# Kernel optimization log

Measured on AMD Instinct MI355X. Metric: run time of the kernel, lower is better.

Reference implementation:

```python
import jax, jax.numpy as jnp
import numpy as np

N, E, G = 50000, 1600000, 64          # nodes, edges, graphs
NODE_IN, EDGE_IN, HID, L, H = 32, 16, 64, 3, 4
C = HID // H                           # per-head channels (PyG out_channels)


def setup_inputs() -> dict:
    key = jax.random.key(0)
    ks = jax.random.split(key, 12)
    x = jax.random.normal(ks[0], (N, NODE_IN), jnp.float32)
    edge_index = jax.random.randint(ks[1], (2, E), 0, N, jnp.int32)
    edge_attr = jax.random.normal(ks[2], (E, EDGE_IN), jnp.float32)
    batch = jnp.sort(jax.random.randint(ks[3], (N,), 0, G, jnp.int32))
    s = lambda k, shape, fan: jax.random.normal(k, shape, jnp.float32) / np.sqrt(fan)
    Wn = s(ks[4], (NODE_IN, HID), NODE_IN); bn = jnp.zeros((HID,), jnp.float32)
    Wq = s(ks[5], (L, HID, HID), HID);      bq = jnp.zeros((L, HID), jnp.float32)
    Wk = s(ks[6], (L, HID, HID), HID);      bk = jnp.zeros((L, HID), jnp.float32)
    Wv = s(ks[7], (L, HID, HID), HID);      bv = jnp.zeros((L, HID), jnp.float32)
    We = s(ks[8], (L, EDGE_IN, HID), EDGE_IN)          # lin_edge, bias=False in PyG
    Ws = s(ks[9], (L, HID, HID), HID);      bs = jnp.zeros((L, HID), jnp.float32)  # lin_skip
    W1 = s(ks[10], (HID, HID // 2), HID);   b1 = jnp.zeros((HID // 2,), jnp.float32)
    W2 = s(ks[11], (HID // 2, 1), HID // 2); b2 = jnp.zeros((1,), jnp.float32)
    return dict(x=x, edge_index=edge_index, edge_attr=edge_attr, batch=batch,
                Wn=Wn, bn=bn, Wq=Wq, bq=bq, Wk=Wk, bk=bk, Wv=Wv, bv=bv,
                We=We, Ws=Ws, bs=bs, W1=W1, b1=b1, W2=W2, b2=b2)


def _transformer_conv(x, src, dst, edge_attr, Wq, bq, Wk, bk, Wv, bv, We, Ws, bs):
    # PyG TransformerConv (concat=True, beta=False, root_weight=True), eval mode.
    q = (x @ Wq + bq)[dst].reshape(E, H, C)              # query at target nodes
    e = (edge_attr @ We).reshape(E, H, C)                # edge embedding
    k = (x @ Wk + bk)[src].reshape(E, H, C) + e          # key at source + edge
    alpha = (q * k).sum(-1) / jnp.sqrt(jnp.float32(C))   # [E, H]
    amax = jax.ops.segment_max(alpha, dst, num_segments=N)
    ex = jnp.exp(alpha - amax[dst])
    denom = jax.ops.segment_sum(ex, dst, num_segments=N)
    attn = ex / (denom[dst] + 1e-16)                     # segment softmax over in-edges
    v = (x @ Wv + bv)[src].reshape(E, H, C) + e
    agg = jax.ops.segment_sum((v * attn[..., None]).reshape(E, HID), dst, num_segments=N)
    return agg + x @ Ws + bs                             # skip connection (lin_skip)


def reference(x, edge_index, edge_attr, batch, Wn, bn, Wq, bq, Wk, bk, Wv, bv,
              We, Ws, bs, W1, b1, W2, b2):
    src, dst = edge_index[0], edge_index[1]
    h = jax.nn.relu(x @ Wn + bn)
    for l in range(L):  # dropout is identity in eval mode
        h_new = jax.nn.relu(_transformer_conv(h, src, dst, edge_attr,
                                              Wq[l], bq[l], Wk[l], bk[l],
                                              Wv[l], bv[l], We[l], Ws[l], bs[l]))
        h = h + h_new
    # global_mean_pool
    cnt = jax.ops.segment_sum(jnp.ones((N,), h.dtype), batch, num_segments=G)
    pooled = jax.ops.segment_sum(h, batch, num_segments=G) / jnp.maximum(cnt, 1.0)[:, None]
    out = jax.nn.relu(pooled @ W1 + b1) @ W2 + b2
    return out.squeeze(-1)
```

## Files before the change

kernel.cpp:

```cpp
#include <hip/hip_runtime.h>
#include <hip/hip_fp16.h>
#include <stdint.h>

#define Nn 50000
#define Ee 1600000
#define Gg 64
#define TB 2048
#define NTB ((Ee + TB - 1) / TB)
#define NBK ((Nn + 255) / 256)

__global__ void k_hist(const int* __restrict__ ei, int* __restrict__ deg) {
    int e = blockIdx.x * blockDim.x + threadIdx.x;
    if (e < Ee) atomicAdd(&deg[ei[Ee + e]], 1);
}

__global__ void k_scan1(const int* __restrict__ deg, int* __restrict__ row_ptr,
                        int* __restrict__ bsum) {
    __shared__ int buf[256];
    int i = blockIdx.x * 256 + threadIdx.x;
    int v = (i < Nn) ? deg[i] : 0;
    buf[threadIdx.x] = v;
    __syncthreads();
    for (int off = 1; off < 256; off <<= 1) {
        int t = (threadIdx.x >= off) ? buf[threadIdx.x - off] : 0;
        __syncthreads();
        buf[threadIdx.x] += t;
        __syncthreads();
    }
    if (i < Nn) row_ptr[i + 1] = buf[threadIdx.x];
    if (threadIdx.x == 255) bsum[blockIdx.x] = buf[255];
}

__global__ void k_scan2(int* __restrict__ bsum, int nb) {
    __shared__ int buf[256];
    int v = (threadIdx.x < nb) ? bsum[threadIdx.x] : 0;
    buf[threadIdx.x] = v;
    __syncthreads();
    for (int off = 1; off < 256; off <<= 1) {
        int t = (threadIdx.x >= off) ? buf[threadIdx.x - off] : 0;
        __syncthreads();
        buf[threadIdx.x] += t;
        __syncthreads();
    }
    if (threadIdx.x < nb) bsum[threadIdx.x] = buf[threadIdx.x];
}

__global__ void k_scan3(int* __restrict__ row_ptr, const int* __restrict__ bsum) {
    int i = blockIdx.x * 256 + threadIdx.x;
    if (i > Nn) return;
    if (i == 0) { row_ptr[0] = 0; return; }
    int b = (i - 1) >> 8;
    if (b > 0) row_ptr[i] += bsum[b - 1];
}

__global__ void k_scatter(const int* __restrict__ ei, int* __restrict__ cursor,
                          int* __restrict__ src_perm, int* __restrict__ eperm) {
    int e = blockIdx.x * blockDim.x + threadIdx.x;
    if (e >= Ee) return;
    int dst = ei[Ee + e];
    int pos = atomicAdd(&cursor[dst], 1);
    src_perm[pos] = ei[e];
    eperm[pos] = e;
}

__global__ void k_easort(const float* __restrict__ ea, const int* __restrict__ eperm,
                         __half* __restrict__ ea_h) {
    long t = (long)blockIdx.x * blockDim.x + threadIdx.x;
    if (t >= (long)Ee * 4) return;
    long idx = t >> 2;
    int e = eperm[idx];
    float4 v = ((const float4*)ea)[(long)e * 4 + (t & 3)];
    __half2 lo = __floats2half2_rn(v.x, v.y);
    __half2 hi = __floats2half2_rn(v.z, v.w);
    ((__half2*)ea_h)[t * 2]     = lo;
    ((__half2*)ea_h)[t * 2 + 1] = hi;
}


__global__ __launch_bounds__(256) void k_cnt(const int* __restrict__ ei,
                                             int* __restrict__ table) {
    __shared__ int hist[NBK];
    for (int i = threadIdx.x; i < NBK; i += 256) hist[i] = 0;
    __syncthreads();
    int e0 = blockIdx.x * TB;
    for (int i = threadIdx.x; i < TB; i += 256) {
        int e = e0 + i;
        if (e >= Ee) break;
        atomicAdd(&hist[ei[Ee + e] >> 8], 1);
    }
    __syncthreads();
    for (int i = threadIdx.x; i < NBK; i += 256)
        table[i * NTB + blockIdx.x] = hist[i];
}

__global__ __launch_bounds__(256) void k_colscan(int* __restrict__ table,
                                                 int* __restrict__ bktsz) {
    __shared__ int buf[1024];
    int c = blockIdx.x;
    for (int k = 0; k < 4; ++k) {
        int i = threadIdx.x + k * 256;
        buf[i] = (i < NTB) ? table[c * NTB + i] : 0;
    }
    __syncthreads();
    for (int off = 1; off < 1024; off <<= 1) {
        int v[4];
        for (int k = 0; k < 4; ++k) {
            int i = threadIdx.x + k * 256;
            v[k] = (i >= off) ? buf[i - off] : 0;
        }
        __syncthreads();
        for (int k = 0; k < 4; ++k) buf[threadIdx.x + k * 256] += v[k];
        __syncthreads();
    }
    for (int k = 0; k < 4; ++k) {
        int i = threadIdx.x + k * 256;
        if (i < NTB) table[c * NTB + i] = i ? buf[i - 1] : 0;
    }
    if (threadIdx.x == 0) bktsz[c] = buf[1023];
}

__global__ __launch_bounds__(256) void k_bktscan(const int* __restrict__ bktsz,
                                                 int* __restrict__ bktbase) {
    __shared__ int buf[256];
    int i = threadIdx.x;
    buf[i] = (i < NBK) ? bktsz[i] : 0;
    __syncthreads();
    for (int off = 1; off < 256; off <<= 1) {
        int v = (i >= off) ? buf[i - off] : 0;
        __syncthreads();
        buf[i] += v;
        __syncthreads();
    }
    if (i == 0) bktbase[0] = 0;
    if (i < NBK) bktbase[i + 1] = buf[i];
}

__global__ __launch_bounds__(256) void k_binfill(const int* __restrict__ ei,
                        const int* __restrict__ table, const int* __restrict__ bktbase,
                        unsigned long long* __restrict__ tmp) {
    __shared__ int off_s[NBK];
    __shared__ int cnt_s[NBK];
    for (int i = threadIdx.x; i < NBK; i += 256) {
        off_s[i] = table[i * NTB + blockIdx.x];
        cnt_s[i] = 0;
    }
    __syncthreads();
    int e0 = blockIdx.x * TB;
    for (int i = threadIdx.x; i < TB; i += 256) {
        int e = e0 + i;
        if (e >= Ee) break;
        int src = ei[e];
        int dst = ei[Ee + e];
        int b = dst >> 8;
        int r = atomicAdd(&cnt_s[b], 1);
        long pos = (long)bktbase[b] + off_s[b] + r;
        tmp[pos] = ((unsigned long long)(unsigned)dst << 37)
                 | ((unsigned long long)(unsigned)src << 21)
                 | (unsigned long long)(unsigned)e;
    }
}

__global__ __launch_bounds__(256) void k_bktB(const unsigned long long* __restrict__ tmp,
                        const int* __restrict__ bktbase, int* __restrict__ row_ptr,
                        unsigned long long* __restrict__ tmp2) {
    __shared__ int cnt[256];
    __shared__ int sc[256];
    __shared__ int lro[256];
    int b = blockIdx.x, tid = threadIdx.x;
    cnt[tid] = 0;
    __syncthreads();
    int s = bktbase[b], t_end = bktbase[b + 1];
    for (int i = s + tid; i < t_end; i += 256)
        atomicAdd(&cnt[(int)(tmp[i] >> 37) & 255], 1);
    __syncthreads();
    sc[tid] = cnt[tid];
    __syncthreads();
    for (int off = 1; off < 256; off <<= 1) {
        int v = (tid >= off) ? sc[tid - off] : 0;
        __syncthreads();
        sc[tid] += v;
        __syncthreads();
    }
    lro[tid] = tid ? sc[tid - 1] : 0;
    cnt[tid] = 0;
    int n = b * 256 + tid;
    if (n < Nn) row_ptr[n] = s + lro[tid];
    if (b == NBK - 1 && tid == 0) row_ptr[Nn] = Ee;
    __syncthreads();
    for (int i = s + tid; i < t_end; i += 256) {
        unsigned long long p = tmp[i];
        int dn = (int)(p >> 37) & 255;
        int r = atomicAdd(&cnt[dn], 1);
        int pos = s + lro[dn] + r;
        tmp2[pos] = (((p >> 21) & 0xFFFFull) << 32) | (p & 0x1FFFFFull);
    }
}

__global__ void k_scatB(const unsigned long long* __restrict__ tmp2,
                        int* __restrict__ src_perm,
                        const float* __restrict__ ea, __half* __restrict__ ea_h) {
    int t = blockIdx.x * blockDim.x + threadIdx.x;
    if (t >= Ee) return;
    unsigned long long p = tmp2[t];
    src_perm[t] = (int)(p >> 32);
    int e = (int)(p & 0xFFFFFFFFull);
    const float4* er = (const float4*)(ea + (size_t)e * 16);
    float4 v0 = er[0], v1 = er[1], v2 = er[2], v3 = er[3];
    __half2 h0 = __floats2half2_rn(v0.x, v0.y), h1 = __floats2half2_rn(v0.z, v0.w);
    __half2 h2 = __floats2half2_rn(v1.x, v1.y), h3 = __floats2half2_rn(v1.z, v1.w);
    __half2 h4 = __floats2half2_rn(v2.x, v2.y), h5 = __floats2half2_rn(v2.z, v2.w);
    __half2 h6 = __floats2half2_rn(v3.x, v3.y), h7 = __floats2half2_rn(v3.z, v3.w);
    uint4 a = make_uint4(*(unsigned*)&h0, *(unsigned*)&h1,
                         *(unsigned*)&h2, *(unsigned*)&h3);
    uint4 bb = make_uint4(*(unsigned*)&h4, *(unsigned*)&h5,
                          *(unsigned*)&h6, *(unsigned*)&h7);
    uint4* o = (uint4*)(ea_h + (size_t)t * 16);
    o[0] = a;
    o[1] = bb;
}

__global__ void k_gbound(const int* __restrict__ batch, int* __restrict__ gstart) {
    int n = blockIdx.x * blockDim.x + threadIdx.x;
    if (n >= Nn) return;
    int b = batch[n];
    if (n == 0) { for (int g = 0; g <= b; ++g) gstart[g] = 0; }
    else { int bp = batch[n - 1]; for (int g = bp + 1; g <= b; ++g) gstart[g] = n; }
    if (n == Nn - 1) { for (int g = b + 1; g <= Gg; ++g) gstart[g] = Nn; }
}

__global__ __launch_bounds__(256) void k_encode(const float* __restrict__ x,
                         const float* __restrict__ Wn,
                         const float* __restrict__ bn, float* __restrict__ h) {
    __shared__ float sx[64 * 32];
    int base = blockIdx.x * 64;
    for (int i = threadIdx.x; i < 512; i += 256) {
        int off = i * 4, row = off >> 5;
        float4 v = (base + row < Nn) ? ((const float4*)(x))[(base * 32 + off) >> 2]
                                     : make_float4(0.f, 0.f, 0.f, 0.f);
        ((float4*)sx)[i] = v;
    }
    __syncthreads();
    int lane = threadIdx.x & 63, wv = threadIdx.x >> 6;
    float acc[16];
    float b = bn[lane];
#pragma unroll
    for (int nn = 0; nn < 16; ++nn) acc[nn] = b;
#pragma unroll 1
    for (int k0 = 0; k0 < 32; k0 += 4) {
        float w0 = Wn[(k0 + 0) * 64 + lane];
        float w1 = Wn[(k0 + 1) * 64 + lane];
        float w2 = Wn[(k0 + 2) * 64 + lane];
        float w3 = Wn[(k0 + 3) * 64 + lane];
#pragma unroll
        for (int nn = 0; nn < 16; ++nn) {
            int row = wv * 16 + nn;
            float4 hv = *(const float4*)&sx[row * 32 + k0];
            acc[nn] = fmaf(hv.x, w0, fmaf(hv.y, w1, fmaf(hv.z, w2, fmaf(hv.w, w3, acc[nn]))));
        }
    }
#pragma unroll
    for (int nn = 0; nn < 16; ++nn) {
        int n = base + wv * 16 + nn;
        if (n < Nn) h[(size_t)n * 64 + lane] = fmaxf(acc[nn], 0.f);
    }
}

__global__ void k_wqm3(const float* __restrict__ Wq_all, const float* __restrict__ bq_all,
                       const float* __restrict__ We_all, float* __restrict__ Wqm3,
                       float* __restrict__ bqm3) {
    int l = blockIdx.x;
    const float* Wq = Wq_all + l * 4096;
    const float* bq = bq_all + l * 64;
    const float* We = We_all + l * 1024;
    float* Wqm = Wqm3 + l * 4096;
    float* bqm = bqm3 + l * 64;
    for (int o = threadIdx.x; o < 64 * 64; o += 256) {
        int j = o >> 6, lp = o & 63, hh = lp >> 4, ii = lp & 15;
        float acc = 0.f;
#pragma unroll
        for (int c = 0; c < 16; ++c)
            acc += Wq[j * 64 + hh * 16 + c] * We[ii * 64 + hh * 16 + c];
        Wqm[o] = acc;
    }
    if (threadIdx.x < 64) {
        int hh = threadIdx.x >> 4, ii = threadIdx.x & 15;
        float acc = 0.f;
#pragma unroll
        for (int c = 0; c < 16; ++c)
            acc += bq[hh * 16 + c] * We[ii * 64 + hh * 16 + c];
        bqm[threadIdx.x] = acc;
    }
}

__global__ __launch_bounds__(256) void k_qkvt(const float* __restrict__ h,
                       const float* __restrict__ Wq, const float* __restrict__ bq,
                       const float* __restrict__ Wk, const float* __restrict__ bk,
                       const float* __restrict__ Wv, const float* __restrict__ bv,
                       const float* __restrict__ Wqm, const float* __restrict__ bqm,
                       const float* __restrict__ Ws, const float* __restrict__ bs,
                       float* __restrict__ qn, __half* __restrict__ kv,
                       float* __restrict__ tq, float* __restrict__ sn) {
    __shared__ float sh[64 * 64];
    int base = blockIdx.x * 64;
    for (int i = threadIdx.x; i < 1024; i += 256) {
        int off = i * 4, row = off >> 6;
        float4 v = (base + row < Nn) ? ((const float4*)(h))[((size_t)base * 64 + off) >> 2]
                                     : make_float4(0.f, 0.f, 0.f, 0.f);
        ((float4*)sh)[i] = v;
    }
    __syncthreads();
    int lane = threadIdx.x & 63, wv = threadIdx.x >> 6;
    float aq[16], ak[16], av[16], at[16], as_[16];
    float _bq = bq[lane], _bk = bk[lane], _bv = bv[lane], _bt = bqm[lane], _bs = bs[lane];
#pragma unroll
    for (int nn = 0; nn < 16; ++nn) {
        aq[nn] = _bq; ak[nn] = _bk; av[nn] = _bv; at[nn] = _bt; as_[nn] = _bs;
    }
#pragma unroll 1
    for (int k0 = 0; k0 < 64; k0 += 4) {
        float wq[4], wk[4], wvv[4], wt[4], ws[4];
#pragma unroll
        for (int j = 0; j < 4; ++j) {
            wq[j] = Wq[(k0 + j) * 64 + lane];
            wk[j] = Wk[(k0 + j) * 64 + lane];
            wvv[j] = Wv[(k0 + j) * 64 + lane];
            wt[j] = Wqm[(k0 + j) * 64 + lane];
            ws[j] = Ws[(k0 + j) * 64 + lane];
        }
#pragma unroll
        for (int nn = 0; nn < 16; ++nn) {
            int row = wv * 16 + nn;
            float4 hv = *(const float4*)&sh[row * 64 + k0];
            aq[nn] = fmaf(hv.x, wq[0], fmaf(hv.y, wq[1], fmaf(hv.z, wq[2], fmaf(hv.w, wq[3], aq[nn]))));
            ak[nn] = fmaf(hv.x, wk[0], fmaf(hv.y, wk[1], fmaf(hv.z, wk[2], fmaf(hv.w, wk[3], ak[nn]))));
            av[nn] = fmaf(hv.x, wvv[0], fmaf(hv.y, wvv[1], fmaf(hv.z, wvv[2], fmaf(hv.w, wvv[3], av[nn]))));
            at[nn] = fmaf(hv.x, wt[0], fmaf(hv.y, wt[1], fmaf(hv.z, wt[2], fmaf(hv.w, wt[3], at[nn]))));
            as_[nn] = fmaf(hv.x, ws[0], fmaf(hv.y, ws[1], fmaf(hv.z, ws[2], fmaf(hv.w, ws[3], as_[nn]))));
        }
    }
#pragma unroll
    for (int nn = 0; nn < 16; ++nn) {
        int n = base + wv * 16 + nn;
        if (n < Nn) {
            size_t o = (size_t)n * 64 + lane;
            qn[o] = aq[nn]; tq[o] = at[nn]; sn[o] = as_[nn];
            kv[(size_t)n * 128 + lane]      = __float2half_rn(ak[nn]);
            kv[(size_t)n * 128 + 64 + lane] = __float2half_rn(av[nn]);
        }
    }
}

__global__ __launch_bounds__(256) void k_layer2(float* __restrict__ h,
                      const float* __restrict__ qn, const __half* __restrict__ kv,
                      const float* __restrict__ tq, const float* __restrict__ sn,
                      const int* __restrict__ row_ptr, const int* __restrict__ src_perm,
                      const __half* __restrict__ eah, const float* __restrict__ We) {
    __shared__ float sWe[1024];
    __shared__ float tE[4][64];
    __shared__ float tV[4][64];
    for (int t = threadIdx.x; t < 1024; t += 256) sWe[t] = We[t];
    __syncthreads();
    int lane = threadIdx.x & 63, wv = threadIdx.x >> 6;
    int slot = lane >> 5, sl = lane & 31;
    int n = blockIdx.x * 4 + wv;
    if (n >= Nn) return;
    int beg = row_ptr[n], end = row_ptr[n + 1];
    const float SC = 0.25f * 1.4426950408889634f;
    float2 q2 = *(const float2*)&qn[(size_t)n * 64 + 2 * sl];
    float2 t2 = *(const float2*)&tq[(size_t)n * 64 + 2 * sl];
    q2.x *= SC; q2.y *= SC; t2.x *= SC; t2.y *= SC;
    const __half2* kv2 = (const __half2*)kv;
    const __half2* ea2 = (const __half2*)eah;
    float m = -INFINITY, accd = 0.f;
    float2 accv = make_float2(0.f, 0.f), acce = make_float2(0.f, 0.f);
    for (int idx = beg; idx < end; idx += 4) {
        int e0 = idx + slot, e1 = idx + 2 + slot;
        bool ok0 = e0 < end, ok1 = e1 < end;
        int i0 = ok0 ? e0 : beg, i1 = ok1 ? e1 : beg;
        int s0 = src_perm[i0], s1 = src_perm[i1];
        float2 k0 = __half22float2(kv2[s0 * 64 + sl]);
        float2 v0 = __half22float2(kv2[s0 * 64 + 32 + sl]);
        float2 k1 = __half22float2(kv2[s1 * 64 + sl]);
        float2 v1 = __half22float2(kv2[s1 * 64 + 32 + sl]);
        float2 x0 = __half22float2(ea2[(size_t)i0 * 8 + (sl & 7)]);
        float2 x1 = __half22float2(ea2[(size_t)i1 * 8 + (sl & 7)]);
        float a0 = fmaf(q2.x, k0.x, fmaf(q2.y, k0.y, fmaf(t2.x, x0.x, t2.y * x0.y)));
        float a1 = fmaf(q2.x, k1.x, fmaf(q2.y, k1.y, fmaf(t2.x, x1.x, t2.y * x1.y)));
        a0 += __shfl_xor(a0, 1, 8); a1 += __shfl_xor(a1, 1, 8);
        a0 += __shfl_xor(a0, 2, 8); a1 += __shfl_xor(a1, 2, 8);
        a0 += __shfl_xor(a0, 4, 8); a1 += __shfl_xor(a1, 4, 8);
        if (!ok0) a0 = -INFINITY;
        if (!ok1) a1 = -INFINITY;
        float b0 = __shfl_xor(a0, 32), b1 = __shfl_xor(a1, 32);
        float nm = fmaxf(m, fmaxf(fmaxf(a0, b0), fmaxf(a1, b1)));
        float w = __builtin_exp2f(m - nm);
        float p0 = __builtin_exp2f(a0 - nm), p1 = __builtin_exp2f(a1 - nm);
        accd = fmaf(accd, w, p0 + p1);
        accv.x = fmaf(accv.x, w, fmaf(p0, v0.x, p1 * v1.x));
        accv.y = fmaf(accv.y, w, fmaf(p0, v0.y, p1 * v1.y));
        acce.x = fmaf(acce.x, w, fmaf(p0, x0.x, p1 * x1.x));
        acce.y = fmaf(acce.y, w, fmaf(p0, x0.y, p1 * x1.y));
        m = nm;
    }
    accd   += __shfl_xor(accd, 32);
    accv.x += __shfl_xor(accv.x, 32);
    accv.y += __shfl_xor(accv.y, 32);
    acce.x += __shfl_xor(acce.x, 32);
    acce.y += __shfl_xor(acce.y, 32);
    float inv = 1.f / (accd + 1e-16f);
    if (slot == 0) {
        ((float2*)tE[wv])[sl] = make_float2(acce.x * inv, acce.y * inv);
        ((float2*)tV[wv])[sl] = make_float2(accv.x * inv, accv.y * inv);
    }
    int hh = lane >> 4;
    float re = 0.f;
#pragma unroll
    for (int i = 0; i < 16; ++i)
        re = fmaf(tE[wv][hh * 16 + i], sWe[i * 64 + lane], re);
    size_t o = (size_t)n * 64 + lane;
    float hv = h[o];
    h[o] = hv + fmaxf(tV[wv][lane] + re + sn[o], 0.f);
}

template <bool SORTED>
__global__ __launch_bounds__(256) void k_layer(float* __restrict__ h,
                      const float* __restrict__ qn, const __half* __restrict__ kv,
                      const float* __restrict__ tq, const float* __restrict__ sn,
                      const int* __restrict__ row_ptr, const int* __restrict__ src_perm,
                      const int* __restrict__ eperm, const __half* __restrict__ eah,
                      const float* __restrict__ eaf, const float* __restrict__ We) {
    __shared__ float sWe[1024];
    __shared__ float tile[4][64];
    for (int t = threadIdx.x; t < 1024; t += 256) sWe[t] = We[t];
    __syncthreads();
    int lane = threadIdx.x & 63, wv = threadIdx.x >> 6;
    int hh = lane >> 4, cc = lane & 15;
    int n = blockIdx.x * 4 + wv;
    if (n >= Nn) return;
    int beg = row_ptr[n], end = row_ptr[n + 1];
    const float SC = 0.25f * 1.4426950408889634f;
    float q = qn[(size_t)n * 64 + lane] * SC;
    float t = tq[(size_t)n * 64 + lane] * SC;
    float m = -INFINITY, accd = 0.f, accv = 0.f, acce = 0.f;
    int idx = beg;
    for (; idx < end; ++idx) {
        long b0 = (long)src_perm[idx] * 128;
        float k0 = __half2float(kv[b0 + lane]);
        float v0 = __half2float(kv[b0 + 64 + lane]);
        float x0 = SORTED ? __half2float(eah[(long)idx * 16 + cc])
                          : eaf[(long)eperm[idx] * 16 + cc];
        float a0 = fmaf(q, k0, x0 * t);
        a0 += __shfl_xor(a0, 1, 16);
        a0 += __shfl_xor(a0, 2, 16);
        a0 += __shfl_xor(a0, 4, 16);
        a0 += __shfl_xor(a0, 8, 16);
        float nm = fmaxf(m, a0);
        float w = __builtin_exp2f(m - nm);
        float p0 = __builtin_exp2f(a0 - nm);
        accd = fmaf(accd, w, p0);
        accv = fmaf(accv, w, p0 * v0);
        acce = fmaf(acce, w, p0 * x0);
        m = nm;
    }
    float inv = 1.f / (accd + 1e-16f);
    tile[wv][lane] = acce * inv;
    float re = 0.f;
#pragma unroll
    for (int i = 0; i < 16; ++i)
        re = fmaf(tile[wv][hh * 16 + i], sWe[i * 64 + lane], re);
    size_t o = (size_t)n * 64 + lane;
    float hv = h[o];
    h[o] = hv + fmaxf(fmaf(accv, inv, re + sn[o]), 0.f);
}

__global__ void k_pool(const float* __restrict__ h, const int* __restrict__ gstart,
                       const float* __restrict__ W1, const float* __restrict__ b1,
                       const float* __restrict__ W2, const float* __restrict__ b2,
                       float* __restrict__ out) {
    int g = blockIdx.x;
    int lane = threadIdx.x & 63, wv = threadIdx.x >> 6;
    int beg = gstart[g], end = gstart[g + 1];
    __shared__ float red[4][64];
    __shared__ float sp[64];
    __shared__ float sh[32];
    float acc = 0.f;
    for (int n = beg + wv; n < end; n += 4) acc += h[(size_t)n * 64 + lane];
    red[wv][lane] = acc;
    __syncthreads();
    if (threadIdx.x < 64) {
        float c = fmaxf((float)(end - beg), 1.f);
        sp[lane] = (red[0][lane] + red[1][lane] + red[2][lane] + red[3][lane]) / c;
    }
    __syncthreads();
    if (threadIdx.x < 32) {
        int t = threadIdx.x;
        float a = b1[t];
#pragma unroll
        for (int i = 0; i < 64; ++i) a = fmaf(sp[i], W1[i * 32 + t], a);
        sh[t] = fmaxf(a, 0.f) * W2[t];
    }
    __syncthreads();
    if (threadIdx.x == 0) {
        float s = b2[0];
#pragma unroll
        for (int i = 0; i < 32; ++i) s += sh[i];
        out[g] = s;
    }
}

extern "C" void kernel_launch(void* const* d_in, const int* in_sizes, int n_in,
                              void* d_out, int out_size, void* d_ws, size_t ws_size,
                              hipStream_t stream) {
    const float* x   = (const float*)d_in[0];
    const int*   ei  = (const int*)d_in[1];
    const float* ea  = (const float*)d_in[2];
    const int*   bat = (const int*)d_in[3];
    const float* Wn  = (const float*)d_in[4];
    const float* bn  = (const float*)d_in[5];
    const float* Wq  = (const float*)d_in[6];
    const float* bq  = (const float*)d_in[7];
    const float* Wk  = (const float*)d_in[8];
    const float* bk  = (const float*)d_in[9];
    const float* Wv  = (const float*)d_in[10];
    const float* bv  = (const float*)d_in[11];
    const float* We  = (const float*)d_in[12];
    const float* Wsk = (const float*)d_in[13];
    const float* bs  = (const float*)d_in[14];
    const float* W1  = (const float*)d_in[15];
    const float* b1  = (const float*)d_in[16];
    const float* W2  = (const float*)d_in[17];
    const float* b2  = (const float*)d_in[18];
    float* out = (float*)d_out;

    const size_t NH = (size_t)Nn * 64;
    float* h    = (float*)d_ws;
    float* qn   = h + NH;
    float* tq   = h + 2 * NH;
    float* sn   = h + 3 * NH;
    __half* kv  = (__half*)(h + 4 * NH);
    float* Wqm3 = h + 5 * NH;
    float* bqm3 = Wqm3 + 3 * 4096;
    int* deg       = (int*)(bqm3 + 3 * 64);
    int* row_ptr   = deg + Nn;
    int* cursor    = row_ptr + Nn + 1;
    int* src_perm  = cursor + Nn;
    int* eperm     = src_perm + Ee;
    int* bsum      = eperm + Ee;
    int* gstart    = bsum + 256;
    char* pe = (char*)(gstart + Gg + 1);
    __half* ea_h = (__half*)(((uintptr_t)pe + 63) & ~(uintptr_t)63);
    char* pt = (char*)(ea_h + (size_t)Ee * 16);
    unsigned long long* tmp =
        (unsigned long long*)(((uintptr_t)pt + 15) & ~(uintptr_t)15);
    size_t need_eah = ((char*)(ea_h + (size_t)Ee * 16)) - (char*)d_ws;
    size_t need_tmp = ((char*)(tmp + Ee)) - (char*)d_ws;
    unsigned long long* tmp2 = (unsigned long long*)qn;
    int* table   = (int*)tq;
    int* bktsz   = (int*)sn;
    int* bktbase = bktsz + 256;
    int mode = (ws_size >= need_tmp) ? 2 : (ws_size >= need_eah) ? 1 : 0;

    if (mode == 2) {
        k_cnt<<<NTB, 256, 0, stream>>>(ei, table);
        k_colscan<<<NBK, 256, 0, stream>>>(table, bktsz);
        k_bktscan<<<1, 256, 0, stream>>>(bktsz, bktbase);
        k_binfill<<<NTB, 256, 0, stream>>>(ei, table, bktbase, tmp);
        k_bktB<<<NBK, 256, 0, stream>>>(tmp, bktbase, row_ptr, tmp2);
        k_scatB<<<(Ee + 255) / 256, 256, 0, stream>>>(tmp2, src_perm, ea, ea_h);
    } else {
        const int NB = 196;
        hipMemsetAsync(deg, 0, Nn * sizeof(int), stream);
        k_hist<<<(Ee + 255) / 256, 256, 0, stream>>>(ei, deg);
        k_scan1<<<NB, 256, 0, stream>>>(deg, row_ptr, bsum);
        k_scan2<<<1, 256, 0, stream>>>(bsum, NB);
        k_scan3<<<(Nn + 256) / 256, 256, 0, stream>>>(row_ptr, bsum);
        hipMemcpyAsync(cursor, row_ptr, Nn * sizeof(int), hipMemcpyDeviceToDevice, stream);
        k_scatter<<<(Ee + 255) / 256, 256, 0, stream>>>(ei, cursor, src_perm, eperm);
        if (mode == 1)
            k_easort<<<((long)Ee * 4 + 255) / 256, 256, 0, stream>>>(ea, eperm, ea_h);
    }
    k_gbound<<<(Nn + 255) / 256, 256, 0, stream>>>(bat, gstart);
    k_wqm3<<<3, 256, 0, stream>>>(Wq, bq, We, Wqm3, bqm3);

    int nodeBlocks = (Nn + 63) / 64;
    k_encode<<<nodeBlocks, 256, 0, stream>>>(x, Wn, bn, h);
    for (int l = 0; l < 3; ++l) {
        k_qkvt<<<nodeBlocks, 256, 0, stream>>>(h, Wq + l * 4096, bq + l * 64,
                                               Wk + l * 4096, bk + l * 64,
                                               Wv + l * 4096, bv + l * 64,
                                               Wqm3 + l * 4096, bqm3 + l * 64,
                                               Wsk + l * 4096, bs + l * 64,
                                               qn, kv, tq, sn);
        if (mode >= 1)
            k_layer2<<<(Nn + 3) / 4, 256, 0, stream>>>(h, qn, kv, tq, sn,
                    row_ptr, src_perm, ea_h, We + l * 1024);
        else
            k_layer<false><<<(Nn + 3) / 4, 256, 0, stream>>>(h, qn, kv, tq, sn,
                    row_ptr, src_perm, eperm, ea_h, ea, We + l * 1024);
    }
    k_pool<<<Gg, 256, 0, stream>>>(h, gstart, W1, b1, W2, b2, out);
}
```

Measured before the change: 725.2 us.

## Process eight edges per wave with fp16 dot2 and max-free softmax

Rewrites the per-node attention kernel so each edge uses 16 lanes with 4-wide fp16 loads of key, value and edge features. A wave now handles 8 edges per iteration instead of 4. Attention logits are computed with packed fp16 dot2 instructions on fp16-rounded queries. The online running-max rescaling is replaced by a fixed exponent offset of -6, which removes the max and rescale work per step. In exchange, the scores lose precision and exp2 can overflow or underflow if logits fall far outside the expected range.

```diff
diff --git a/kernel.cpp b/kernel.cpp
--- a/kernel.cpp
+++ b/kernel.cpp
@@ -8,6 +8,17 @@
 #define TB 2048
 #define NTB ((Ee + TB - 1) / TB)
 #define NBK ((Nn + 255) / 256)
+
+typedef _Float16 f16x2 __attribute__((ext_vector_type(2)));
+typedef _Float16 f16x4 __attribute__((ext_vector_type(4)));
+
+__device__ __forceinline__ float fdot2f(f16x2 a, f16x2 b, float c) {
+#if __has_builtin(__builtin_amdgcn_fdot2)
+    return __builtin_amdgcn_fdot2(a, b, c, false);
+#else
+    return fmaf((float)a[0], (float)b[0], fmaf((float)a[1], (float)b[1], c));
+#endif
+}
 
 __global__ void k_hist(const int* __restrict__ ei, int* __restrict__ deg) {
     int e = blockIdx.x * blockDim.x + threadIdx.x;
@@ -350,7 +361,7 @@
     }
 }
 
-__global__ __launch_bounds__(256) void k_layer2(float* __restrict__ h,
+__global__ __launch_bounds__(256) void k_layer4(float* __restrict__ h,
                       const float* __restrict__ qn, const __half* __restrict__ kv,
                       const float* __restrict__ tq, const float* __restrict__ sn,
                       const int* __restrict__ row_ptr, const int* __restrict__ src_perm,
@@ -361,56 +372,69 @@
     for (int t = threadIdx.x; t < 1024; t += 256) sWe[t] = We[t];
     __syncthreads();
     int lane = threadIdx.x & 63, wv = threadIdx.x >> 6;
-    int slot = lane >> 5, sl = lane & 31;
+    int slot = lane >> 4, sl = lane & 15;
     int n = blockIdx.x * 4 + wv;
     if (n >= Nn) return;
     int beg = row_ptr[n], end = row_ptr[n + 1];
     const float SC = 0.25f * 1.4426950408889634f;
-    float2 q2 = *(const float2*)&qn[(size_t)n * 64 + 2 * sl];
-    float2 t2 = *(const float2*)&tq[(size_t)n * 64 + 2 * sl];
-    q2.x *= SC; q2.y *= SC; t2.x *= SC; t2.y *= SC;
-    const __half2* kv2 = (const __half2*)kv;
-    const __half2* ea2 = (const __half2*)eah;
-    float m = -INFINITY, accd = 0.f;
-    float2 accv = make_float2(0.f, 0.f), acce = make_float2(0.f, 0.f);
-    for (int idx = beg; idx < end; idx += 4) {
-        int e0 = idx + slot, e1 = idx + 2 + slot;
+    float4 q4 = *(const float4*)&qn[(size_t)n * 64 + 4 * sl];
+    float4 t4 = *(const float4*)&tq[(size_t)n * 64 + 4 * sl];
+    f16x2 qa = {(_Float16)(q4.x * SC), (_Float16)(q4.y * SC)};
+    f16x2 qb = {(_Float16)(q4.z * SC), (_Float16)(q4.w * SC)};
+    f16x2 ta = {(_Float16)(t4.x * SC), (_Float16)(t4.y * SC)};
+    f16x2 tb = {(_Float16)(t4.z * SC), (_Float16)(t4.w * SC)};
+    const int xoff = 4 * (sl & 3);
+    float accd = 0.f;
+    float4 accv = make_float4(0.f, 0.f, 0.f, 0.f);
+    float4 acce = make_float4(0.f, 0.f, 0.f, 0.f);
+    for (int idx = beg; idx < end; idx += 8) {
+        int e0 = idx + slot, e1 = idx + 4 + slot;
         bool ok0 = e0 < end, ok1 = e1 < end;
         int i0 = ok0 ? e0 : beg, i1 = ok1 ? e1 : beg;
         int s0 = src_perm[i0], s1 = src_perm[i1];
-        float2 k0 = __half22float2(kv2[s0 * 64 + sl]);
-        float2 v0 = __half22float2(kv2[s0 * 64 + 32 + sl]);
-        float2 k1 = __half22float2(kv2[s1 * 64 + sl]);
-        float2 v1 = __half22float2(kv2[s1 * 64 + 32 + sl]);
-        float2 x0 = __half22float2(ea2[(size_t)i0 * 8 + (sl & 7)]);
-        float2 x1 = __half22float2(ea2[(size_t)i1 * 8 + (sl & 7)]);
-        float a0 = fmaf(q2.x, k0.x, fmaf(q2.y, k0.y, fmaf(t2.x, x0.x, t2.y * x0.y)));
-        float a1 = fmaf(q2.x, k1.x, fmaf(q2.y, k1.y, fmaf(t2.x, x1.x, t2.y * x1.y)));
-        a0 += __shfl_xor(a0, 1, 8); a1 += __shfl_xor(a1, 1, 8);
-        a0 += __shfl_xor(a0, 2, 8); a1 += __shfl_xor(a1, 2, 8);
-        a0 += __shfl_xor(a0, 4, 8); a1 += __shfl_xor(a1, 4, 8);
-        if (!ok0) a0 = -INFINITY;
-        if (!ok1) a1 = -INFINITY;
-        float b0 = __shfl_xor(a0, 32), b1 = __shfl_xor(a1, 32);
-        float nm = fmaxf(m, fmaxf(fmaxf(a0, b0), fmaxf(a1, b1)));
-        float w = __builtin_exp2f(m - nm);
-        float p0 = __builtin_exp2f(a0 - nm), p1 = __builtin_exp2f(a1 - nm);
-        accd = fmaf(accd, w, p0 + p1);
-        accv.x = fmaf(accv.x, w, fmaf(p0, v0.x, p1 * v1.x));
-        accv.y = fmaf(accv.y, w, fmaf(p0, v0.y, p1 * v1.y));
-        acce.x = fmaf(acce.x, w, fmaf(p0, x0.x, p1 * x1.x));
-        acce.y = fmaf(acce.y, w, fmaf(p0, x0.y, p1 * x1.y));
-        m = nm;
-    }
-    accd   += __shfl_xor(accd, 32);
-    accv.x += __shfl_xor(accv.x, 32);
-    accv.y += __shfl_xor(accv.y, 32);
-    acce.x += __shfl_xor(acce.x, 32);
-    acce.y += __shfl_xor(acce.y, 32);
+        f16x4 k0 = *(const f16x4*)(kv + (size_t)s0 * 128 + 4 * sl);
+        f16x4 v0 = *(const f16x4*)(kv + (size_t)s0 * 128 + 64 + 4 * sl);
+        f16x4 k1 = *(const f16x4*)(kv + (size_t)s1 * 128 + 4 * sl);
+        f16x4 v1 = *(const f16x4*)(kv + (size_t)s1 * 128 + 64 + 4 * sl);
+        f16x4 x0 = *(const f16x4*)(eah + (size_t)i0 * 16 + xoff);
+        f16x4 x1 = *(const f16x4*)(eah + (size_t)i1 * 16 + xoff);
+        float a0 = fdot2f(qa, __builtin_shufflevector(k0, k0, 0, 1),
+                   fdot2f(qb, __builtin_shufflevector(k0, k0, 2, 3),
+                   fdot2f(ta, __builtin_shufflevector(x0, x0, 0, 1),
+                   fdot2f(tb, __builtin_shufflevector(x0, x0, 2, 3), -6.0f))));
+        float a1 = fdot2f(qa, __builtin_shufflevector(k1, k1, 0, 1),
+                   fdot2f(qb, __builtin_shufflevector(k1, k1, 2, 3),
+                   fdot2f(ta, __builtin_shufflevector(x1, x1, 0, 1),
+                   fdot2f(tb, __builtin_shufflevector(x1, x1, 2, 3), -6.0f))));
+        a0 += __shfl_xor(a0, 1, 4); a1 += __shfl_xor(a1, 1, 4);
+        a0 += __shfl_xor(a0, 2, 4); a1 += __shfl_xor(a1, 2, 4);
+        float p0 = ok0 ? __builtin_exp2f(a0) : 0.f;
+        float p1 = ok1 ? __builtin_exp2f(a1) : 0.f;
+        accd += p0 + p1;
+        accv.x = fmaf(p0, (float)v0[0], fmaf(p1, (float)v1[0], accv.x));
+        accv.y = fmaf(p0, (float)v0[1], fmaf(p1, (float)v1[1], accv.y));
+        accv.z = fmaf(p0, (float)v0[2], fmaf(p1, (float)v1[2], accv.z));
+        accv.w = fmaf(p0, (float)v0[3], fmaf(p1, (float)v1[3], accv.w));
+        acce.x = fmaf(p0, (float)x0[0], fmaf(p1, (float)x1[0], acce.x));
+        acce.y = fmaf(p0, (float)x0[1], fmaf(p1, (float)x1[1], acce.y));
+        acce.z = fmaf(p0, (float)x0[2], fmaf(p1, (float)x1[2], acce.z));
+        acce.w = fmaf(p0, (float)x0[3], fmaf(p1, (float)x1[3], acce.w));
+    }
+    accd   += __shfl_xor(accd, 16);   accd   += __shfl_xor(accd, 32);
+    accv.x += __shfl_xor(accv.x, 16); accv.x += __shfl_xor(accv.x, 32);
+    accv.y += __shfl_xor(accv.y, 16); accv.y += __shfl_xor(accv.y, 32);
+    accv.z += __shfl_xor(accv.z, 16); accv.z += __shfl_xor(accv.z, 32);
+    accv.w += __shfl_xor(accv.w, 16); accv.w += __shfl_xor(accv.w, 32);
+    acce.x += __shfl_xor(acce.x, 16); acce.x += __shfl_xor(acce.x, 32);
+    acce.y += __shfl_xor(acce.y, 16); acce.y += __shfl_xor(acce.y, 32);
+    acce.z += __shfl_xor(acce.z, 16); acce.z += __shfl_xor(acce.z, 32);
+    acce.w += __shfl_xor(acce.w, 16); acce.w += __shfl_xor(acce.w, 32);
     float inv = 1.f / (accd + 1e-16f);
     if (slot == 0) {
-        ((float2*)tE[wv])[sl] = make_float2(acce.x * inv, acce.y * inv);
-        ((float2*)tV[wv])[sl] = make_float2(accv.x * inv, accv.y * inv);
+        ((float4*)tE[wv])[sl] = make_float4(acce.x * inv, acce.y * inv,
+                                            acce.z * inv, acce.w * inv);
+        ((float4*)tV[wv])[sl] = make_float4(accv.x * inv, accv.y * inv,
+                                            accv.z * inv, accv.w * inv);
     }
     int hh = lane >> 4;
     float re = 0.f;
@@ -592,7 +616,7 @@
                                                Wsk + l * 4096, bs + l * 64,
                                                qn, kv, tq, sn);
         if (mode >= 1)
-            k_layer2<<<(Nn + 3) / 4, 256, 0, stream>>>(h, qn, kv, tq, sn,
+            k_layer4<<<(Nn + 3) / 4, 256, 0, stream>>>(h, qn, kv, tq, sn,
                     row_ptr, src_perm, ea_h, We + l * 1024);
         else
             k_layer<false><<<(Nn + 3) / 4, 256, 0, stream>>>(h, qn, kv, tq, sn,
```

New measurement: 681.4 us. -6.0%, faster.
